# Optimization experiments

Measured on AMD Instinct MI355X. Metric: run time of the kernel, lower is better.

Reference implementation:

```python
import jax, jax.numpy as jnp
import numpy as np

B, S, D = 4, 2048, 768
H = 12
DH = D // H
NUM_WAY = 4
DFF = 4 * D  # FFN expansion scale=4
EPS = 1e-6


def setup_inputs() -> dict:
    key = jax.random.key(0)
    ks = jax.random.split(key, 20)
    s = 0.02
    inp = {
        "x": jax.random.normal(ks[0], (B, S, D), jnp.float32),
        "w": jax.random.randint(ks[1], (B, S), 0, NUM_WAY, jnp.int64),
        # LayerNorm 1
        "ln1_g": jnp.ones((D,), jnp.float32),
        "ln1_b": jnp.zeros((D,), jnp.float32),
        # Multi-head attention projections (input_dim=out_dim=D)
        "wq": jax.random.normal(ks[2], (D, D), jnp.float32) * s,
        "bq": jnp.zeros((D,), jnp.float32),
        "wk": jax.random.normal(ks[3], (D, D), jnp.float32) * s,
        "bk": jnp.zeros((D,), jnp.float32),
        "wv": jax.random.normal(ks[4], (D, D), jnp.float32) * s,
        "bv": jnp.zeros((D,), jnp.float32),
        "wo": jax.random.normal(ks[5], (D, D), jnp.float32) * s,
        "bo": jnp.zeros((D,), jnp.float32),
        # Way classifier
        "wcls": jax.random.normal(ks[6], (D, NUM_WAY), jnp.float32) * s,
        "bcls": jnp.zeros((NUM_WAY,), jnp.float32),
        # num_way stacked FFN experts: Linear(D,4D) -> ReLU -> Linear(4D,D)
        "w1": jax.random.normal(ks[7], (NUM_WAY, D, DFF), jnp.float32) * s,
        "b1": jnp.zeros((NUM_WAY, DFF), jnp.float32),
        "w2": jax.random.normal(ks[8], (NUM_WAY, DFF, D), jnp.float32) * s,
        "b2": jnp.zeros((NUM_WAY, D), jnp.float32),
    }
    return inp


def _layernorm(x, g, b):
    mu = jnp.mean(x, axis=-1, keepdims=True)
    var = jnp.mean(jnp.square(x - mu), axis=-1, keepdims=True)
    return (x - mu) * jax.lax.rsqrt(var + EPS) * g + b


def reference(x, w, ln1_g, ln1_b, wq, bq, wk, bk, wv, bv, wo, bo,
              wcls, bcls, w1, b1, w2, b2):
    # pre-LN
    xn = _layernorm(x, ln1_g, ln1_b)
    # multi-head self-attention (q = k = v = xn)
    q = (xn @ wq + bq).reshape(B, S, H, DH)
    k = (xn @ wk + bk).reshape(B, S, H, DH)
    v = (xn @ wv + bv).reshape(B, S, H, DH)
    scores = jnp.einsum('bqhd,bkhd->bhqk', q, k) / jnp.sqrt(jnp.float32(DH))
    attn = jax.nn.softmax(scores, axis=-1)
    ctx = jnp.einsum('bhqk,bkhd->bqhd', attn, v).reshape(B, S, D)
    ctx = ctx @ wo + bo
    # dropout is identity at inference; residual
    out = ctx + x
    # dense compute-all-experts FFN, then per-token select by routing id w
    # (mask-overwrite in original == one-hot select since masks partition)
    ffn_out = jnp.zeros_like(out)
    for ci in range(NUM_WAY):
        h = jax.nn.relu(out @ w1[ci] + b1[ci])        # [B,S,4D]
        fi = h @ w2[ci] + b2[ci]                      # [B,S,D]
        mask = (w == ci).astype(out.dtype)[..., None]  # [B,S,1]
        if ci == 0:
            # original initializes ffn_out with way-0 output everywhere;
            # later ways overwrite where w == ci, net = select expert w
            ffn_out = fi
        else:
            ffn_out = ffn_out * (1.0 - mask) + fi * mask
    way_logits = out @ wcls + bcls  # [B,S,NUM_WAY]
    return ffn_out, way_logits
```

## Files before the change

### kernel.cpp

```cpp
#include <hip/hip_runtime.h>
#include <cstdint>

typedef unsigned short u16;
typedef float f32x4 __attribute__((ext_vector_type(4)));
typedef float f32x16 __attribute__((ext_vector_type(16)));
typedef __bf16 bf16x8 __attribute__((ext_vector_type(8)));

#define LOG2E 1.44269504088896340736f

__device__ __forceinline__ u16 f2bf(float f) {
    union { float f; unsigned u; } v; v.f = f;
    unsigned r = v.u + 0x7fffu + ((v.u >> 16) & 1u);
    return (u16)(r >> 16);
}

__device__ __forceinline__ float bf2f(u16 v) {
    union { unsigned u; float f; } x; x.u = ((unsigned)v) << 16; return x.f;
}

__device__ __forceinline__ unsigned cvt_pk_bf16(float lo, float hi) {
    unsigned r;
    asm("v_cvt_pk_bf16_f32 %0, %1, %2" : "=v"(r) : "v"(lo), "v"(hi));
    return r;
}

__device__ __forceinline__ float exp2_hw(float x) {
    float r;
    asm("v_exp_f32 %0, %1" : "=v"(r) : "v"(x));
    return r;
}

__device__ __forceinline__ f32x4 mfma16(bf16x8 a, bf16x8 b, f32x4 c) {
    return __builtin_amdgcn_mfma_f32_16x16x32_bf16(a, b, c, 0, 0, 0);
}

__device__ __forceinline__ f32x16 mfma32(bf16x8 a, bf16x8 b, f32x16 c) {
    return __builtin_amdgcn_mfma_f32_32x32x16_bf16(a, b, c, 0, 0, 0);
}

__device__ __forceinline__ void gload_lds16(const void* g, void* l) {
    __builtin_amdgcn_global_load_lds(
        (__attribute__((address_space(1))) unsigned int*)(g),
        (__attribute__((address_space(3))) unsigned int*)(l),
        16, 0, 0);
}

#define MB_TOK 8192
#define DM 768
#define HH 12
#define DHD 64
#define NWAY 4
#define DFF 3072
#define SEQ 2048
#define NBATCH 4

#define PREP_LN_END   8192
#define PREP_T7_END   10496
#define PREP_W1_END   19712
#define PREP_W2_END   28928
#define PREP_CB_END   28937
#define PREP_GRID     28938

__global__ __launch_bounds__(256) void prep_kernel(
    const float* __restrict__ x, const float* __restrict__ ln_g,
    const float* __restrict__ ln_b, u16* __restrict__ xn,
    const float* __restrict__ wq, const float* __restrict__ wk,
    const float* __restrict__ wvv, const float* __restrict__ wo,
    u16* __restrict__ wqkvt, u16* __restrict__ wot,
    const float* __restrict__ w1, u16* __restrict__ w1t,
    const float* __restrict__ w2, u16* __restrict__ w2t,
    const float* __restrict__ bq, const float* __restrict__ bk,
    const float* __restrict__ bv, float* __restrict__ bqkv,
    const int* __restrict__ wl, int* __restrict__ perm,
    int* __restrict__ eoff, int4* __restrict__ fmap, int4* __restrict__ fmap64)
{
    __shared__ float tl[32][33];
    __shared__ float red[4];
    __shared__ int cnt[4], cur[4], off[5];
    int bid = blockIdx.x, tid = threadIdx.x;

    if (bid < PREP_LN_END) {
        int row = bid;
        const float* xr = x + (size_t)row * DM;
        float v0 = xr[tid], v1 = xr[tid + 256], v2 = xr[tid + 512];
        float s = v0 + v1 + v2;
        #pragma unroll
        for (int k = 1; k < 64; k <<= 1) s += __shfl_xor(s, k);
        if ((tid & 63) == 0) red[tid >> 6] = s;
        __syncthreads();
        float mu = (red[0] + red[1] + red[2] + red[3]) * (1.f / 768.f);
        float d0 = v0 - mu, d1 = v1 - mu, d2 = v2 - mu;
        float q = d0 * d0 + d1 * d1 + d2 * d2;
        #pragma unroll
        for (int k = 1; k < 64; k <<= 1) q += __shfl_xor(q, k);
        __syncthreads();
        if ((tid & 63) == 0) red[tid >> 6] = q;
        __syncthreads();
        float var = (red[0] + red[1] + red[2] + red[3]) * (1.f / 768.f);
        float rs = rsqrtf(var + 1e-6f);
        u16* xo = xn + (size_t)row * DM;
        xo[tid]       = f2bf(d0 * rs * ln_g[tid]       + ln_b[tid]);
        xo[tid + 256] = f2bf(d1 * rs * ln_g[tid + 256] + ln_b[tid + 256]);
        xo[tid + 512] = f2bf(d2 * rs * ln_g[tid + 512] + ln_b[tid + 512]);
        return;
    }
    if (bid < PREP_W2_END) {
        const float* src; u16* dst; int K, N, n0, k0;
        if (bid < PREP_T7_END) {
            int r = bid - PREP_LN_END;
            int wsel = r / 576, lb = r % 576;
            K = 768; N = 768;
            n0 = (lb % 24) * 32; k0 = (lb / 24) * 32;
            src = wsel == 0 ? wq : (wsel == 1 ? wk : (wsel == 2 ? wvv : wo));
            dst = wsel == 3 ? wot : (wqkvt + (size_t)wsel * 768 * 768);
        } else if (bid < PREP_W1_END) {
            int lb = bid - PREP_T7_END;
            K = 768; N = 3072;
            n0 = (lb % 96) * 32; k0 = ((lb / 96) % 24) * 32;
            int z = lb / 2304;
            src = w1 + (size_t)z * K * N; dst = w1t + (size_t)z * K * N;
        } else {
            int lb = bid - PREP_W1_END;
            K = 3072; N = 768;
            n0 = (lb % 24) * 32; k0 = ((lb / 24) % 96) * 32;
            int z = lb / 2304;
            src = w2 + (size_t)z * K * N; dst = w2t + (size_t)z * K * N;
        }
        int tx = tid & 31, ty = tid >> 5;
        #pragma unroll
        for (int j = 0; j < 4; ++j)
            tl[ty + j * 8][tx] = src[(size_t)(k0 + ty + j * 8) * N + n0 + tx];
        __syncthreads();
        #pragma unroll
        for (int j = 0; j < 4; ++j)
            dst[(size_t)(n0 + ty + j * 8) * K + k0 + tx] = f2bf(tl[tx][ty + j * 8]);
        return;
    }
    if (bid < PREP_CB_END) {
        int i = (bid - PREP_W2_END) * 256 + tid;
        if (i < 2304)
            bqkv[i] = i < 768 ? bq[i] : (i < 1536 ? bk[i - 768] : bv[i - 1536]);
        return;
    }
    if (tid < 4) cnt[tid] = 0;
    __syncthreads();
    for (int t = tid; t < MB_TOK; t += 256) atomicAdd(&cnt[wl[t] & 3], 1);
    __syncthreads();
    if (tid == 0) {
        off[0] = 0;
        for (int e = 0; e < 4; ++e) off[e + 1] = off[e] + cnt[e];
        int idx = 0;
        for (int e = 0; e < 4; ++e)
            for (int s = 0; s < cnt[e]; s += 128)
                fmap[idx++] = make_int4(e, off[e], s, cnt[e] - s);
        for (; idx < 72; ++idx) fmap[idx] = make_int4(-1, 0, 0, 0);
        int idx2 = 0;
        for (int e = 0; e < 4; ++e)
            for (int s = 0; s < cnt[e]; s += 64)
                fmap64[idx2++] = make_int4(e, off[e], s, cnt[e] - s);
        for (; idx2 < 144; ++idx2) fmap64[idx2] = make_int4(-1, 0, 0, 0);
        for (int e = 0; e < 5; ++e) eoff[e] = off[e];
        for (int e = 0; e < 4; ++e) cur[e] = off[e];
    }
    __syncthreads();
    for (int t = tid; t < MB_TOK; t += 256) {
        int e = wl[t] & 3;
        int pos = atomicAdd(&cur[e], 1);
        perm[pos] = t;
    }
}

__global__ __launch_bounds__(256) void vT_kernel(
    const u16* __restrict__ qkv, u16* __restrict__ vT)
{
    __shared__ u16 tl[32][33];
    int bh = blockIdx.z;
    int b = bh / HH, h = bh % HH;
    int key0 = blockIdx.x * 32;
    int d0 = blockIdx.y * 32;
    int tx = threadIdx.x & 31, ty = threadIdx.x >> 5;
    const u16* src = qkv + ((size_t)b * SEQ + key0) * 2304 + 1536 + h * 64 + d0;
    #pragma unroll
    for (int j = 0; j < 4; ++j)
        tl[ty + j * 8][tx] = src[(size_t)(ty + j * 8) * 2304 + tx];
    __syncthreads();
    u16* dst = vT + ((size_t)bh * 64 + d0) * SEQ + key0;
    #pragma unroll
    for (int j = 0; j < 4; ++j)
        dst[(size_t)(ty + j * 8) * SEQ + tx] = tl[tx][ty + j * 8];
}

template<int MODE, int TM, int TN, int GCH, bool RELU, bool RES, bool ST32, bool ST16>
__global__ __launch_bounds__(256, (TM == 64) ? (TN == 64 ? 8 : 6) : 5)
void gemm_bt_kernel(
    const u16* __restrict__ A, const u16* __restrict__ Bt,
    const float* __restrict__ bias, const float* __restrict__ res,
    float* __restrict__ out32, u16* __restrict__ out16,
    int nbt, int N, int K, int ntn,
    const int* __restrict__ perm, const int4* __restrict__ fmap)
{
    constexpr int ALD = TM * 32;
    constexpr int BLD = TN * 32;
    constexpr int NN  = (TM == 128) ? (TN / 32) : (TN / 64);
    __shared__ __attribute__((aligned(16))) u16 As[2][ALD];
    __shared__ __attribute__((aligned(16))) u16 Bs[2][BLD];
    int tid = threadIdx.x;
    int wv = tid >> 6, ln = tid & 63;
    int bpx = gridDim.x / (ntn << 3);
    int jj = blockIdx.x >> 3;
    int bt, tn;
    if (GCH > 0) {
        int pc = GCH * ntn;
        int chunk = jj / pc, rem = jj % pc;
        bt = (blockIdx.x & 7) * bpx + chunk * GCH + rem % GCH;
        tn = (rem / GCH) * TN;
    } else {
        bt = (blockIdx.x & 7) * bpx + jj / ntn;
        tn = (jj % ntn) * TN;
    }
    if (bt >= nbt) return;

    int seg = 0, ms = 0, mb = TM, tm = 0;
    if (MODE != 0) {
        int4 ent = fmap[bt];
        if (ent.x < 0) return;
        seg = ent.y; ms = ent.z; mb = ent.w; if (mb > TM) mb = TM;
        Bt += (size_t)ent.x * N * K;
        bias += ent.x * N;
    } else {
        tm = bt * TM;
    }

    f32x4 acc[4][NN];
    #pragma unroll
    for (int i = 0; i < 4; ++i)
        #pragma unroll
        for (int j = 0; j < NN; ++j) acc[i][j] = f32x4{0.f, 0.f, 0.f, 0.f};

    int wr = (TM == 128) ? (wv >> 1) : 0;
    int wcol0 = (TM == 128) ? (wv & 1) * (TN / 2) : wv * (TN / 4);
    int lr = ln & 15, hi = ln >> 4;
    int nk = K / 32;

    const u16* asrc[2];
    const u16* bsrc[2];
    #pragma unroll
    for (int i = 0; i < 2; ++i) {
        int rA = (TM == 128) ? ((wv * 2 + i) * 16 + (ln >> 2))
                             : (wv * 16 + (ln >> 2));
        if (TM == 128 || i == 0) {
            int am = rA < mb ? rA : (mb - 1);
            size_t arow;
            if (MODE == 1)      arow = (size_t)perm[seg + ms + am];
            else if (MODE == 2) arow = (size_t)(seg + ms + am);
            else                arow = (size_t)(tm + rA);
            int colA = (((ln & 3) ^ ((rA >> 1) & 3))) * 8;
            asrc[i] = A + arow * K + colA;
        }
        int rB = (TN == 128) ? ((wv * 2 + i) * 16 + (ln >> 2))
                             : (wv * 16 + (ln >> 2));
        if (TN == 128 || i == 0) {
            int colB = (((ln & 3) ^ ((rB >> 1) & 3))) * 8;
            bsrc[i] = Bt + (size_t)(tn + rB) * K + colB;
        }
    }
    int aofs0 = (TM == 128) ? (wv * 2) * 512 : wv * 512;
    int bofs0 = (TN == 128) ? (wv * 2) * 512 : wv * 512;
    int sw = (lr >> 1) & 3;

#define GSTAGE(bf_, k0_) do {                                             \
    gload_lds16(asrc[0] + (k0_), &As[bf_][aofs0]);                        \
    if (TM == 128) gload_lds16(asrc[1] + (k0_), &As[bf_][aofs0 + 512]);   \
    gload_lds16(bsrc[0] + (k0_), &Bs[bf_][bofs0]);                        \
    if (TN == 128) gload_lds16(bsrc[1] + (k0_), &Bs[bf_][bofs0 + 512]);   \
} while (0)

    GSTAGE(0, 0);
    for (int kk = 0; kk < nk; ++kk) {
        int bf = kk & 1;
        __syncthreads();
        if (kk + 1 < nk) GSTAGE(bf ^ 1, (kk + 1) * 32);
        bf16x8 a[4], b[NN];
        #pragma unroll
        for (int m = 0; m < 4; ++m)
            a[m] = *(const bf16x8*)&As[bf][(wr * 64 + m * 16 + lr) * 32 + (hi ^ sw) * 8];
        #pragma unroll
        for (int n = 0; n < NN; ++n)
            b[n] = *(const bf16x8*)&Bs[bf][(wcol0 + n * 16 + lr) * 32 + (hi ^ sw) * 8];
        #pragma unroll
        for (int m = 0; m < 4; ++m)
            #pragma unroll
            for (int n = 0; n < NN; ++n)
                acc[m][n] = mfma16(a[m], b[n], acc[m][n]);
    }
#undef GSTAGE

    #pragma unroll
    for (int m = 0; m < 4; ++m) {
        int rb = wr * 64 + m * 16 + hi * 4;
        #pragma unroll
        for (int n = 0; n < NN; ++n) {
            int gcol = tn + wcol0 + n * 16 + lr;
            float bvv = bias[gcol];
            #pragma unroll
            for (int i = 0; i < 4; ++i) {
                int rml = rb + i;
                float v = acc[m][n][i] + bvv;
                if (RELU) v = v > 0.f ? v : 0.f;
                if (MODE == 0) {
                    size_t grow = (size_t)(tm + rml);
                    if (RES) v += res[grow * N + gcol];
                    if (ST32) out32[grow * N + gcol] = v;
                    if (ST16) out16[grow * N + gcol] = f2bf(v);
                } else {
                    if (rml < mb) {
                        size_t orow = (MODE == 1) ? (size_t)(seg + ms + rml)
                                                  : (size_t)perm[seg + ms + rml];
                        if (ST32) out32[orow * N + gcol] = v;
                        if (ST16) out16[orow * N + gcol] = f2bf(v);
                    }
                }
            }
        }
    }
}

__global__ __launch_bounds__(256, 4) void attn_kernel(
    const u16* __restrict__ qkv, const u16* __restrict__ vT,
    u16* __restrict__ ctx)
{
    __shared__ __attribute__((aligned(16))) u16 Ks[2][4096];
    __shared__ __attribute__((aligned(16))) u16 Vs[2][4096];
    int tid = threadIdx.x;
    int wv = tid >> 6, ln = tid & 63;
    int qv = ln & 31, hi = ln >> 5;
    int bid = blockIdx.x;
    int bh = (bid & 7) * 6 + ((bid >> 3) % 6);
    int qt = (bid >> 3) / 6;
    int b = bh / HH, h = bh % HH;
    int q0 = qt * 128 + wv * 32;
    size_t qrowb = (size_t)(b * SEQ + q0);
    const float C = 0.125f * LOG2E;

    bf16x8 qf[4];
    {
        const u16* qp = qkv + (qrowb + qv) * 2304 + h * 64 + hi * 8;
        #pragma unroll
        for (int ds = 0; ds < 4; ++ds) qf[ds] = *(const bf16x8*)(qp + ds * 16);
    }

    int csrc = 8 * ((ln & 7) ^ (ln >> 3));
    const size_t kbase = (size_t)b * SEQ * 2304 + 768 + h * 64;
    const u16* vtb = vT + (size_t)bh * 64 * SEQ;
    const u16* kp0 = qkv + kbase + (size_t)(wv * 16 + (ln >> 3)) * 2304 + csrc;
    const u16* kp1 = kp0 + (size_t)8 * 2304;
    const u16* vp0 = vtb + (size_t)(wv * 16 + (ln >> 3)) * SEQ + csrc;
    const u16* vp1 = vp0 + (size_t)8 * SEQ;

#define ATTN_STAGE(bf_, t_) do {                                          \
    gload_lds16(kp0 + (size_t)(t_) * 64 * 2304, &Ks[bf_][(wv * 2) * 512]);\
    gload_lds16(kp1 + (size_t)(t_) * 64 * 2304, &Ks[bf_][(wv * 2 + 1) * 512]);\
    gload_lds16(vp0 + (size_t)(t_) * 64, &Vs[bf_][(wv * 2) * 512]);       \
    gload_lds16(vp1 + (size_t)(t_) * 64, &Vs[bf_][(wv * 2 + 1) * 512]);   \
} while (0)

    f32x16 oacc[2];
    #pragma unroll
    for (int i = 0; i < 2; ++i)
        #pragma unroll
        for (int r = 0; r < 16; ++r) oacc[i][r] = 0.f;
    float m_run = -INFINITY, l_run = 0.f;
    int ksw = (qv & 7) * 8;

    ATTN_STAGE(0, 0);

    for (int kt = 0; kt < SEQ / 64; ++kt) {
        int bf = kt & 1;
        __syncthreads();
        if (kt + 1 < SEQ / 64) ATTN_STAGE(bf ^ 1, kt + 1);

        f32x16 s0, s1;
        #pragma unroll
        for (int r = 0; r < 16; ++r) { s0[r] = 0.f; s1[r] = 0.f; }
        #pragma unroll
        for (int ds = 0; ds < 4; ++ds) {
            bf16x8 ka0 = *(const bf16x8*)&Ks[bf][qv * 64 + ((ds * 16 + hi * 8) ^ ksw)];
            bf16x8 ka1 = *(const bf16x8*)&Ks[bf][(32 + qv) * 64 + ((ds * 16 + hi * 8) ^ ksw)];
            s0 = mfma32(ka0, qf[ds], s0);
            s1 = mfma32(ka1, qf[ds], s1);
        }

        float tmax = s0[0];
        #pragma unroll
        for (int r = 1; r < 16; ++r) tmax = fmaxf(tmax, s0[r]);
        #pragma unroll
        for (int r = 0; r < 16; ++r) tmax = fmaxf(tmax, s1[r]);
        tmax = fmaxf(tmax, __shfl_xor(tmax, 32));

        if (!__all(tmax - m_run <= 64.f)) {
            float m_new = fmaxf(m_run, tmax);
            float corr = exp2_hw((m_run - m_new) * C);
            l_run *= corr;
            #pragma unroll
            for (int i = 0; i < 2; ++i)
                #pragma unroll
                for (int r = 0; r < 16; ++r) oacc[i][r] *= corr;
            m_run = m_new;
        }
        float c2 = -m_run * C;
        float psum = 0.f;
        #pragma unroll
        for (int r = 0; r < 16; ++r) {
            s0[r] = exp2_hw(fmaf(s0[r], C, c2)); psum += s0[r];
            s1[r] = exp2_hw(fmaf(s1[r], C, c2)); psum += s1[r];
        }
        l_run += psum;

        #pragma unroll
        for (int kb = 0; kb < 2; ++kb) {
            #pragma unroll
            for (int hc = 0; hc < 2; ++hc) {
                const f32x16& sv = kb ? s1 : s0;
                unsigned x0 = cvt_pk_bf16(sv[8 * hc + 0], sv[8 * hc + 1]);
                unsigned x1 = cvt_pk_bf16(sv[8 * hc + 2], sv[8 * hc + 3]);
                unsigned x2 = cvt_pk_bf16(sv[8 * hc + 4], sv[8 * hc + 5]);
                unsigned x3 = cvt_pk_bf16(sv[8 * hc + 6], sv[8 * hc + 7]);
                unsigned t0 = hi ? x0 : x2, t1 = hi ? x1 : x3;
                unsigned r0 = (unsigned)__shfl_xor((int)t0, 32);
                unsigned r1 = (unsigned)__shfl_xor((int)t1, 32);
                union { bf16x8 v; unsigned u[4]; } pf;
                pf.u[0] = hi ? r0 : x0; pf.u[1] = hi ? r1 : x1;
                pf.u[2] = hi ? x2 : r0; pf.u[3] = hi ? x3 : r1;
                int kc = (kb * 32 + hc * 16 + hi * 8) ^ ksw;
                #pragma unroll
                for (int dblk = 0; dblk < 2; ++dblk) {
                    bf16x8 va = *(const bf16x8*)&Vs[bf][(dblk * 32 + qv) * 64 + kc];
                    oacc[dblk] = mfma32(va, pf.v, oacc[dblk]);
                }
            }
        }
    }
#undef ATTN_STAGE

    float l_tot = l_run + __shfl_xor(l_run, 32);
    float inv = 1.f / l_tot;

    __syncthreads();
    u16* eb = &Ks[0][0] + wv * 2048;
    #pragma unroll
    for (int dblk = 0; dblk < 2; ++dblk)
        #pragma unroll
        for (int r = 0; r < 16; r += 2) {
            int d = dblk * 32 + (r & 3) + 8 * (r >> 2) + 4 * hi;
            unsigned pk = cvt_pk_bf16(oacc[dblk][r] * inv, oacc[dblk][r + 1] * inv);
            *(unsigned*)&eb[qv * 64 + (d ^ ((qv & 7) * 8))] = pk;
        }
    __syncthreads();
    {
        u16* ctr = ctx + (qrowb + qv) * DM + h * 64 + hi * 32;
        #pragma unroll
        for (int g = 0; g < 4; ++g) {
            bf16x8 vv = *(const bf16x8*)&eb[qv * 64 + ((hi * 32 + g * 8) ^ ((qv & 7) * 8))];
            *(bf16x8*)(ctr + g * 8) = vv;
        }
    }
}

__global__ __launch_bounds__(256) void cls_kernel(
    const u16* __restrict__ outm, const float* __restrict__ wcls,
    const float* __restrict__ bcls, float* __restrict__ dst)
{
    int row = blockIdx.x, t = threadIdx.x;
    const u16* xr = outm + (size_t)row * DM;
    float a0 = 0, a1 = 0, a2 = 0, a3 = 0;
    for (int j = t; j < DM; j += 256) {
        float xv = bf2f(xr[j]);
        float4 wv4 = *(const float4*)(const void*)(wcls + (size_t)j * 4);
        a0 += xv * wv4.x; a1 += xv * wv4.y; a2 += xv * wv4.z; a3 += xv * wv4.w;
    }
    #pragma unroll
    for (int k = 1; k < 64; k <<= 1) {
        a0 += __shfl_xor(a0, k); a1 += __shfl_xor(a1, k);
        a2 += __shfl_xor(a2, k); a3 += __shfl_xor(a3, k);
    }
    __shared__ float red[4][4];
    if ((t & 63) == 0) {
        int wid = t >> 6;
        red[wid][0] = a0; red[wid][1] = a1; red[wid][2] = a2; red[wid][3] = a3;
    }
    __syncthreads();
    if (t < 4)
        dst[(size_t)row * 4 + t] =
            red[0][t] + red[1][t] + red[2][t] + red[3][t] + bcls[t];
}

extern "C" void kernel_launch(void* const* d_in, const int* in_sizes, int n_in,
                              void* d_out, int out_size, void* d_ws, size_t ws_size,
                              hipStream_t stream) {
    const float* x      = (const float*)d_in[0];
    const int*   wl     = (const int*)d_in[1];
    const float* ln_g   = (const float*)d_in[2];
    const float* ln_b   = (const float*)d_in[3];
    const float* wq     = (const float*)d_in[4];
    const float* bq     = (const float*)d_in[5];
    const float* wk     = (const float*)d_in[6];
    const float* bk     = (const float*)d_in[7];
    const float* wvv    = (const float*)d_in[8];
    const float* bv     = (const float*)d_in[9];
    const float* wo     = (const float*)d_in[10];
    const float* bo     = (const float*)d_in[11];
    const float* wcls   = (const float*)d_in[12];
    const float* bcls   = (const float*)d_in[13];
    const float* w1     = (const float*)d_in[14];
    const float* b1     = (const float*)d_in[15];
    const float* w2     = (const float*)d_in[16];
    const float* b2     = (const float*)d_in[17];
    float* out = (float*)d_out;

    char* ws = (char*)d_ws;
    u16*   xn    = (u16*)  (ws + 0);
    u16*   qkv   = (u16*)  (ws + 12582912);
    u16*   hbuf  = (u16*)  (ws + 0);
    u16*   ctx   = (u16*)  (ws + 50331648);
    u16*   outb  = (u16*)  (ws + 62914560);
    u16*   wqkvt = (u16*)  (ws + 75497472);
    u16*   wot   = (u16*)  (ws + 79036416);
    u16*   w1t   = (u16*)  (ws + 80216064);
    u16*   w2t   = (u16*)  (ws + 99090432);
    float* bqkv  = (float*)(ws + 117964800);
    int*   perm  = (int*)  (ws + 117974016);
    int*   eoff  = (int*)  (ws + 118006784);
    int4*  fmap  = (int4*) (ws + 118006816);
    int4*  fmap64= (int4*) (ws + 118007968);
    u16*   vT    = (u16*)  (ws + 118010272);

    prep_kernel<<<PREP_GRID, 256, 0, stream>>>(
        x, ln_g, ln_b, xn, wq, wk, wvv, wo, wqkvt, wot,
        w1, w1t, w2, w2t, bq, bk, bv, bqkv, wl, perm, eoff, fmap, fmap64);

    gemm_bt_kernel<0, 128, 128, 0, false, false, false, true><<<1152, 256, 0, stream>>>(
        xn, wqkvt, bqkv, nullptr, nullptr, qkv, 64, 2304, 768, 18, nullptr, nullptr);

    vT_kernel<<<dim3(64, 2, 48), 256, 0, stream>>>(qkv, vT);

    attn_kernel<<<768, 256, 0, stream>>>(qkv, vT, ctx);

    gemm_bt_kernel<0, 64, 64, 0, false, true, false, true><<<1536, 256, 0, stream>>>(
        ctx, wot, bo, x, nullptr, outb, 128, 768, 768, 12, nullptr, nullptr);

    cls_kernel<<<MB_TOK, 256, 0, stream>>>(outb, wcls, bcls, out + (size_t)MB_TOK * DM);

    gemm_bt_kernel<1, 128, 128, 9, true, false, false, true><<<1728, 256, 0, stream>>>(
        outb, w1t, b1, nullptr, nullptr, hbuf, 72, DFF, 768, 24, perm, fmap);

    gemm_bt_kernel<2, 64, 64, 6, false, false, true, false><<<1728, 256, 0, stream>>>(
        hbuf, w2t, b2, nullptr, out, nullptr, 144, 768, DFF, 12, perm, fmap64);
}
```

Before: 379.9 us.

## Add split-K to FFN down-projection GEMM and widen tiles to 64x128

Adds a split-K template parameter to the GEMM. The second FFN GEMM now runs with two K slices and 64x128 tiles, writing partial sums to a scratch buffer that a new elementwise kernel adds into the output. The output projection GEMM also moves to 64x128 tiles with half the grid, and the occupancy hints in launch_bounds are lowered. The aim is better operand reuse per tile while keeping enough blocks in flight for the long-K GEMM. The cost is an extra kernel launch plus a full fp32 read-modify-write pass over the output.

```diff
diff --git a/kernel.cpp b/kernel.cpp
--- a/kernel.cpp
+++ b/kernel.cpp
@@ -190,12 +190,14 @@
         dst[(size_t)(ty + j * 8) * SEQ + tx] = tl[tx][ty + j * 8];
 }
 
-template<int MODE, int TM, int TN, int GCH, bool RELU, bool RES, bool ST32, bool ST16>
-__global__ __launch_bounds__(256, (TM == 64) ? (TN == 64 ? 8 : 6) : 5)
+template<int MODE, int TM, int TN, int GCH, int KS,
+         bool RELU, bool RES, bool ST32, bool ST16>
+__global__ __launch_bounds__(256, (TM == 64) ? 6 : 4)
 void gemm_bt_kernel(
     const u16* __restrict__ A, const u16* __restrict__ Bt,
     const float* __restrict__ bias, const float* __restrict__ res,
-    float* __restrict__ out32, u16* __restrict__ out16,
+    float* __restrict__ out32, float* __restrict__ out32b,
+    u16* __restrict__ out16,
     int nbt, int N, int K, int ntn,
     const int* __restrict__ perm, const int4* __restrict__ fmap)
 {
@@ -206,18 +208,21 @@
     __shared__ __attribute__((aligned(16))) u16 Bs[2][BLD];
     int tid = threadIdx.x;
     int wv = tid >> 6, ln = tid & 63;
-    int bpx = gridDim.x / (ntn << 3);
+    int nin = ntn * KS;
+    int bpx = gridDim.x / (nin << 3);
     int jj = blockIdx.x >> 3;
-    int bt, tn;
+    int bt, inner;
     if (GCH > 0) {
-        int pc = GCH * ntn;
+        int pc = GCH * nin;
         int chunk = jj / pc, rem = jj % pc;
         bt = (blockIdx.x & 7) * bpx + chunk * GCH + rem % GCH;
-        tn = (rem / GCH) * TN;
+        inner = rem / GCH;
     } else {
-        bt = (blockIdx.x & 7) * bpx + jj / ntn;
-        tn = (jj % ntn) * TN;
-    }
+        bt = (blockIdx.x & 7) * bpx + jj / nin;
+        inner = jj % nin;
+    }
+    int tn = (inner % ntn) * TN;
+    int ks = inner / ntn;
     if (bt >= nbt) return;
 
     int seg = 0, ms = 0, mb = TM, tm = 0;
@@ -240,7 +245,8 @@
     int wr = (TM == 128) ? (wv >> 1) : 0;
     int wcol0 = (TM == 128) ? (wv & 1) * (TN / 2) : wv * (TN / 4);
     int lr = ln & 15, hi = ln >> 4;
-    int nk = K / 32;
+    int nk = K / KS / 32;
+    int kbase = ks * (K / KS);
 
     const u16* asrc[2];
     const u16* bsrc[2];
@@ -255,13 +261,13 @@
             else if (MODE == 2) arow = (size_t)(seg + ms + am);
             else                arow = (size_t)(tm + rA);
             int colA = (((ln & 3) ^ ((rA >> 1) & 3))) * 8;
-            asrc[i] = A + arow * K + colA;
+            asrc[i] = A + arow * K + kbase + colA;
         }
         int rB = (TN == 128) ? ((wv * 2 + i) * 16 + (ln >> 2))
                              : (wv * 16 + (ln >> 2));
         if (TN == 128 || i == 0) {
             int colB = (((ln & 3) ^ ((rB >> 1) & 3))) * 8;
-            bsrc[i] = Bt + (size_t)(tn + rB) * K + colB;
+            bsrc[i] = Bt + (size_t)(tn + rB) * K + kbase + colB;
         }
     }
     int aofs0 = (TM == 128) ? (wv * 2) * 512 : wv * 512;
@@ -295,13 +301,14 @@
     }
 #undef GSTAGE
 
+    float* o32 = (KS > 1 && ks != 0) ? out32b : out32;
     #pragma unroll
     for (int m = 0; m < 4; ++m) {
         int rb = wr * 64 + m * 16 + hi * 4;
         #pragma unroll
         for (int n = 0; n < NN; ++n) {
             int gcol = tn + wcol0 + n * 16 + lr;
-            float bvv = bias[gcol];
+            float bvv = (KS > 1 && ks != 0) ? 0.f : bias[gcol];
             #pragma unroll
             for (int i = 0; i < 4; ++i) {
                 int rml = rb + i;
@@ -310,19 +317,29 @@
                 if (MODE == 0) {
                     size_t grow = (size_t)(tm + rml);
                     if (RES) v += res[grow * N + gcol];
-                    if (ST32) out32[grow * N + gcol] = v;
+                    if (ST32) o32[grow * N + gcol] = v;
                     if (ST16) out16[grow * N + gcol] = f2bf(v);
                 } else {
                     if (rml < mb) {
                         size_t orow = (MODE == 1) ? (size_t)(seg + ms + rml)
                                                   : (size_t)perm[seg + ms + rml];
-                        if (ST32) out32[orow * N + gcol] = v;
+                        if (ST32) o32[orow * N + gcol] = v;
                         if (ST16) out16[orow * N + gcol] = f2bf(v);
                     }
                 }
             }
         }
     }
+}
+
+__global__ __launch_bounds__(256) void addred_kernel(
+    const float* __restrict__ p1, float* __restrict__ dst)
+{
+    size_t i = ((size_t)blockIdx.x * 256 + threadIdx.x) * 4;
+    float4 a = *(const float4*)(const void*)(dst + i);
+    float4 b = *(const float4*)(const void*)(p1 + i);
+    a.x += b.x; a.y += b.y; a.z += b.z; a.w += b.w;
+    *(float4*)(void*)(dst + i) = a;
 }
 
 __global__ __launch_bounds__(256, 4) void attn_kernel(
@@ -533,26 +550,37 @@
     int4*  fmap  = (int4*) (ws + 118006816);
     int4*  fmap64= (int4*) (ws + 118007968);
     u16*   vT    = (u16*)  (ws + 118010272);
+    float* pp1   = (float*)(ws + 50331648);
 
     prep_kernel<<<PREP_GRID, 256, 0, stream>>>(
         x, ln_g, ln_b, xn, wq, wk, wvv, wo, wqkvt, wot,
         w1, w1t, w2, w2t, bq, bk, bv, bqkv, wl, perm, eoff, fmap, fmap64);
 
-    gemm_bt_kernel<0, 128, 128, 0, false, false, false, true><<<1152, 256, 0, stream>>>(
-        xn, wqkvt, bqkv, nullptr, nullptr, qkv, 64, 2304, 768, 18, nullptr, nullptr);
+    gemm_bt_kernel<0, 128, 128, 0, 1, false, false, false, true>
+        <<<1152, 256, 0, stream>>>(
+        xn, wqkvt, bqkv, nullptr, nullptr, nullptr, qkv,
+        64, 2304, 768, 18, nullptr, nullptr);
 
     vT_kernel<<<dim3(64, 2, 48), 256, 0, stream>>>(qkv, vT);
 
     attn_kernel<<<768, 256, 0, stream>>>(qkv, vT, ctx);
 
-    gemm_bt_kernel<0, 64, 64, 0, false, true, false, true><<<1536, 256, 0, stream>>>(
-        ctx, wot, bo, x, nullptr, outb, 128, 768, 768, 12, nullptr, nullptr);
+    gemm_bt_kernel<0, 64, 128, 0, 1, false, true, false, true>
+        <<<768, 256, 0, stream>>>(
+        ctx, wot, bo, x, nullptr, nullptr, outb,
+        128, 768, 768, 6, nullptr, nullptr);
 
     cls_kernel<<<MB_TOK, 256, 0, stream>>>(outb, wcls, bcls, out + (size_t)MB_TOK * DM);
 
-    gemm_bt_kernel<1, 128, 128, 9, true, false, false, true><<<1728, 256, 0, stream>>>(
-        outb, w1t, b1, nullptr, nullptr, hbuf, 72, DFF, 768, 24, perm, fmap);
-
-    gemm_bt_kernel<2, 64, 64, 6, false, false, true, false><<<1728, 256, 0, stream>>>(
-        hbuf, w2t, b2, nullptr, out, nullptr, 144, 768, DFF, 12, perm, fmap64);
-}
+    gemm_bt_kernel<1, 128, 128, 9, 1, true, false, false, true>
+        <<<1728, 256, 0, stream>>>(
+        outb, w1t, b1, nullptr, nullptr, nullptr, hbuf,
+        72, DFF, 768, 24, perm, fmap);
+
+    gemm_bt_kernel<2, 64, 128, 6, 2, false, false, true, false>
+        <<<1728, 256, 0, stream>>>(
+        hbuf, w2t, b2, nullptr, out, pp1, nullptr,
+        144, 768, DFF, 6, perm, fmap64);
+
+    addred_kernel<<<6144, 256, 0, stream>>>(pp1, out);
+}
```

Result: faster. 370.5 us (-2.5%).
